# Performance work log

Measured on AMD Instinct MI355X. Metric: run time of the kernel, lower is better.

The kernel has to match this reference:

```python
import jax, jax.numpy as jnp
import numpy as np

S = 14          # grid size
B = 2           # boxes per cell
L_COORD = 5.0
L_NOOBJ = 0.5
N_BATCH = 4096
OBJ_PROB = 0.3  # fraction of cells containing an object


def xywh2xyxy(boxes):
    # boxes [..., 4] with (cx, cy, w, h); cx,cy are in grid units -> divide by S
    x, y, w, h = boxes[..., 0], boxes[..., 1], boxes[..., 2], boxes[..., 3]
    return jnp.stack([x / S - 0.5 * w, y / S - 0.5 * h,
                      x / S + 0.5 * w, y / S + 0.5 * h], axis=-1)


def iou_elementwise(b1, b2):
    # b1, b2: [..., 4] in xyxy format; elementwise IoU (the diagonal of compute_iou)
    lt = jnp.maximum(b1[..., :2], b2[..., :2])
    rb = jnp.minimum(b1[..., 2:], b2[..., 2:])
    wh = jnp.maximum(rb - lt, 0.0)
    inter = wh[..., 0] * wh[..., 1]
    area1 = (b1[..., 2] - b1[..., 0]) * (b1[..., 3] - b1[..., 1])
    area2 = (b2[..., 2] - b2[..., 0]) * (b2[..., 3] - b2[..., 1])
    return inter / (area1 + area2 - inter)


def setup_inputs() -> dict:
    key = jax.random.key(0)
    k1, k2, k3, k4 = jax.random.split(key, 4)
    pred_tensor = jax.random.uniform(k1, (N_BATCH, S, S, 30), dtype=jnp.float32)
    target_boxes = jax.random.uniform(k2, (N_BATCH, S, S, 4), dtype=jnp.float32)
    target_cls = jax.random.uniform(k3, (N_BATCH, S, S, 20), dtype=jnp.float32)
    has_object_map = jax.random.bernoulli(k4, OBJ_PROB, (N_BATCH, S, S))
    return {"pred_tensor": pred_tensor, "target_boxes": target_boxes,
            "target_cls": target_cls, "has_object_map": has_object_map}


def reference(pred_tensor, target_boxes, target_cls, has_object_map):
    N = pred_tensor.shape[0]
    dt = pred_tensor.dtype
    obj = has_object_map.astype(dt)          # (N,S,S)
    noobj = 1.0 - obj
    n_obj = jnp.sum(obj)
    n_noobj = jnp.sum(noobj)

    pred_b1 = pred_tensor[..., 0:5]
    pred_b2 = pred_tensor[..., 5:10]
    pred_cls = pred_tensor[..., 10:30]

    # class prediction loss: sum over object cells / batch size
    cls_loss = jnp.sum(obj[..., None] * (pred_cls - target_cls) ** 2) / N

    # no-object loss: gt confidence (and all 5 entries) assumed 0; per-box sum / num noobj cells
    no_obj_loss = L_NOOBJ * (
        jnp.sum(noobj[..., None] * pred_b1 ** 2) +
        jnp.sum(noobj[..., None] * pred_b2 ** 2)) / n_noobj

    # best-of-B box selection via elementwise IoU against the target box
    tgt_xyxy = xywh2xyxy(target_boxes)
    iou1 = iou_elementwise(xywh2xyxy(pred_b1[..., :4]), tgt_xyxy)
    iou2 = iou_elementwise(xywh2xyxy(pred_b2[..., :4]), tgt_xyxy)
    take1 = iou1 >= iou2
    best_boxes = jnp.where(take1[..., None], pred_b1, pred_b2)  # (N,S,S,5)
    best_iou = jnp.where(take1, iou1, iou2)                      # (N,S,S)

    bx, by, bw, bh = (best_boxes[..., i] for i in range(4))
    tx, ty, tw, th = (target_boxes[..., i] for i in range(4))
    reg = (bx - tx) ** 2 + (by - ty) ** 2 + \
          (jnp.sqrt(bw) - jnp.sqrt(tw)) ** 2 + (jnp.sqrt(bh) - jnp.sqrt(th)) ** 2
    reg_loss = jnp.sum(obj * reg) * L_COORD / n_obj

    # containing-object confidence loss; IoU target is detached
    conf_loss = jnp.sum(
        obj * (best_boxes[..., 4] - jax.lax.stop_gradient(best_iou)) ** 2) / n_obj

    total_loss = reg_loss + conf_loss + no_obj_loss + cls_loss
    return total_loss, reg_loss, conf_loss, no_obj_loss, cls_loss
```

## Files before the change

### kernel.cpp

```cpp
#include <hip/hip_runtime.h>

constexpr int NSLOTS = 64;

__global__ void yl_detect_zero(const unsigned int* __restrict__ hmap,
                               double* __restrict__ acc,
                               int* __restrict__ flag) {
    __shared__ int ok[2];
    const int t = threadIdx.x;
    if (t < 2) ok[t] = 1;
    __syncthreads();
    bool vi = true, vf = true;
    for (int i = t; i < 1024; i += 256) {
        const unsigned int d = hmap[i];
        vi = vi && (d == 0u || d == 1u);
        vf = vf && (d == 0u || d == 0x3f800000u);
    }
    if (!vi) atomicAnd(&ok[0], 0);
    if (!vf) atomicAnd(&ok[1], 0);
    for (int i = t; i < NSLOTS * 5; i += 256) acc[i] = 0.0;
    __syncthreads();
    if (t == 0) *flag = ok[0] ? 1 : (ok[1] ? 2 : 0);
}

__global__ __launch_bounds__(256) void yl_main(
    const float* __restrict__ pred, const float* __restrict__ tb,
    const float* __restrict__ tc, const void* __restrict__ hmap,
    const int* __restrict__ flag_p, double* __restrict__ acc, int cells)
{
    const int cell = blockIdx.x * 256 + threadIdx.x;
    float obj = 0.f, s_cls = 0.f, s_no = 0.f, s_reg = 0.f, s_conf = 0.f;

    if (cell < cells) {
        const int flag = *flag_p;
        if (flag == 1)      obj = (float)((const int*)hmap)[cell];
        else if (flag == 2) obj = ((const float*)hmap)[cell];
        else                obj = (float)((const unsigned char*)hmap)[cell];

        float p[30];
        const float2* p2 = reinterpret_cast<const float2*>(pred + (size_t)cell * 30);
        #pragma unroll
        for (int i = 0; i < 15; ++i) { const float2 v = p2[i]; p[2*i] = v.x; p[2*i+1] = v.y; }

        const float4 tbv = reinterpret_cast<const float4*>(tb)[cell];

        float tcl[20];
        const float4* t4 = reinterpret_cast<const float4*>(tc + (size_t)cell * 20);
        #pragma unroll
        for (int i = 0; i < 5; ++i) {
            const float4 v = t4[i];
            tcl[4*i] = v.x; tcl[4*i+1] = v.y; tcl[4*i+2] = v.z; tcl[4*i+3] = v.w;
        }

        float c = 0.f;
        #pragma unroll
        for (int i = 0; i < 20; ++i) { const float d = p[10 + i] - tcl[i]; c += d * d; }
        s_cls = obj * c;

        float nn = 0.f;
        #pragma unroll
        for (int i = 0; i < 10; ++i) nn += p[i] * p[i];
        s_no = (1.f - obj) * nn;

        const float tx1 = tbv.x / 14.f - 0.5f * tbv.z, ty1 = tbv.y / 14.f - 0.5f * tbv.w;
        const float tx2 = tbv.x / 14.f + 0.5f * tbv.z, ty2 = tbv.y / 14.f + 0.5f * tbv.w;
        const float ta  = (tx2 - tx1) * (ty2 - ty1);

        auto iou_f = [&](float x, float y, float w, float h) -> float {
            const float x1 = x / 14.f - 0.5f * w, y1 = y / 14.f - 0.5f * h;
            const float x2 = x / 14.f + 0.5f * w, y2 = y / 14.f + 0.5f * h;
            const float lw = fmaxf(fminf(x2, tx2) - fmaxf(x1, tx1), 0.f);
            const float lh = fmaxf(fminf(y2, ty2) - fmaxf(y1, ty1), 0.f);
            const float inter = lw * lh;
            const float a = (x2 - x1) * (y2 - y1);
            return inter / (a + ta - inter);
        };
        const float iou1 = iou_f(p[0], p[1], p[2], p[3]);
        const float iou2 = iou_f(p[5], p[6], p[7], p[8]);

        const bool take1 = iou1 >= iou2;
        const float bx = take1 ? p[0] : p[5];
        const float by = take1 ? p[1] : p[6];
        const float bw = take1 ? p[2] : p[7];
        const float bh = take1 ? p[3] : p[8];
        const float bc = take1 ? p[4] : p[9];
        const float biou = take1 ? iou1 : iou2;

        const float dx = bx - tbv.x, dy = by - tbv.y;
        const float dw = sqrtf(bw) - sqrtf(tbv.z);
        const float dh = sqrtf(bh) - sqrtf(tbv.w);
        s_reg = obj * (dx * dx + dy * dy + dw * dw + dh * dh);
        const float dc = bc - biou;
        s_conf = obj * dc * dc;
    }

    float vals[5] = {obj, s_cls, s_no, s_reg, s_conf};
    #pragma unroll
    for (int i = 0; i < 5; ++i) {
        float v = vals[i];
        #pragma unroll
        for (int off = 32; off > 0; off >>= 1) v += __shfl_down(v, off);
        vals[i] = v;
    }
    __shared__ float red[4][5];
    const int lane = threadIdx.x & 63, wid = threadIdx.x >> 6;
    if (lane == 0) {
        #pragma unroll
        for (int i = 0; i < 5; ++i) red[wid][i] = vals[i];
    }
    __syncthreads();
    if (threadIdx.x < 5) {
        const float s = red[0][threadIdx.x] + red[1][threadIdx.x]
                      + red[2][threadIdx.x] + red[3][threadIdx.x];
        atomicAdd(&acc[(blockIdx.x & (NSLOTS - 1)) * 5 + threadIdx.x], (double)s);
    }
}

__global__ void yl_finalize(const double* __restrict__ acc, float* __restrict__ out,
                            int cells, int nbatch) {
    const int t = threadIdx.x;
    double v[5];
    #pragma unroll
    for (int i = 0; i < 5; ++i) v[i] = acc[t * 5 + i];
    #pragma unroll
    for (int i = 0; i < 5; ++i) {
        #pragma unroll
        for (int off = 32; off > 0; off >>= 1) v[i] += __shfl_down(v[i], off);
    }
    if (t == 0) {
        const double n_obj = v[0], n_noobj = (double)cells - v[0];
        const float reg_loss  = (float)(v[3] * 5.0 / n_obj);
        const float conf_loss = (float)(v[4] / n_obj);
        const float no_loss   = (float)(0.5 * v[2] / n_noobj);
        const float cls_loss  = (float)(v[1] / (double)nbatch);
        out[1] = reg_loss;
        out[2] = conf_loss;
        out[3] = no_loss;
        out[4] = cls_loss;
        out[0] = reg_loss + conf_loss + no_loss + cls_loss;
    }
}

extern "C" void kernel_launch(void* const* d_in, const int* in_sizes, int n_in,
                              void* d_out, int out_size, void* d_ws, size_t ws_size,
                              hipStream_t stream) {
    const float* pred = (const float*)d_in[0];
    const float* tb   = (const float*)d_in[1];
    const float* tc   = (const float*)d_in[2];
    const void*  hm   = d_in[3];
    const int cells  = in_sizes[3];
    const int nbatch = cells / 196;
    double* acc = (double*)d_ws;
    int* flag   = (int*)((char*)d_ws + NSLOTS * 5 * sizeof(double));

    yl_detect_zero<<<1, 256, 0, stream>>>((const unsigned int*)hm, acc, flag);
    const int blocks = (cells + 255) / 256;
    yl_main<<<blocks, 256, 0, stream>>>(pred, tb, tc, hm, flag, acc, cells);
    yl_finalize<<<1, 64, 0, stream>>>(acc, (float*)d_out, cells, nbatch);
}
```

Before: 206.8 us.

## Split each cell across five threads for coalesced loads and shared-memory box handoff

Each grid cell is now handled by five cooperating threads, each loading a float2 box slice plus a slice of the class predictions and targets. The box values are staged in shared memory so one thread per cell can do the IoU and regression work. This aims to make the strided per-cell loads better coalesced and raise memory-level parallelism. The cost is 640-thread blocks, an extra barrier, and most threads idling during the IoU phase; the detect kernel's scan bound is also clamped to the input size.

```diff
diff --git a/kernel.cpp b/kernel.cpp
--- a/kernel.cpp
+++ b/kernel.cpp
@@ -4,13 +4,13 @@
 
 __global__ void yl_detect_zero(const unsigned int* __restrict__ hmap,
                                double* __restrict__ acc,
-                               int* __restrict__ flag) {
+                               int* __restrict__ flag, int bound) {
     __shared__ int ok[2];
     const int t = threadIdx.x;
     if (t < 2) ok[t] = 1;
     __syncthreads();
     bool vi = true, vf = true;
-    for (int i = t; i < 1024; i += 256) {
+    for (int i = t; i < bound; i += 256) {
         const unsigned int d = hmap[i];
         vi = vi && (d == 0u || d == 1u);
         vf = vf && (d == 0u || d == 0x3f800000u);
@@ -22,13 +22,21 @@
     if (t == 0) *flag = ok[0] ? 1 : (ok[1] ? 2 : 0);
 }
 
-__global__ __launch_bounds__(256) void yl_main(
+__global__ __launch_bounds__(640) void yl_main(
     const float* __restrict__ pred, const float* __restrict__ tb,
     const float* __restrict__ tc, const void* __restrict__ hmap,
     const int* __restrict__ flag_p, double* __restrict__ acc, int cells)
 {
-    const int cell = blockIdx.x * 256 + threadIdx.x;
+    __shared__ float lp[128 * 10];
+    __shared__ float red[10][5];
+
+    const int tl = threadIdx.x;
+    const int cl = tl / 5;
+    const int q  = tl - 5 * cl;
+    const int cell = blockIdx.x * 128 + cl;
+
     float obj = 0.f, s_cls = 0.f, s_no = 0.f, s_reg = 0.f, s_conf = 0.f;
+    float objsum = 0.f;
 
     if (cell < cells) {
         const int flag = *flag_p;
@@ -36,30 +44,27 @@
         else if (flag == 2) obj = ((const float*)hmap)[cell];
         else                obj = (float)((const unsigned char*)hmap)[cell];
 
-        float p[30];
-        const float2* p2 = reinterpret_cast<const float2*>(pred + (size_t)cell * 30);
+        const float* pc = pred + (size_t)cell * 30;
+        const float2 nb = *reinterpret_cast<const float2*>(pc + 2 * q);
+        const float2 ca = *reinterpret_cast<const float2*>(pc + 10 + 4 * q);
+        const float2 cb = *reinterpret_cast<const float2*>(pc + 12 + 4 * q);
+        const float4 tcv = *reinterpret_cast<const float4*>(tc + (size_t)cell * 20 + 4 * q);
+
+        *reinterpret_cast<float2*>(&lp[cl * 10 + 2 * q]) = nb;
+
+        s_no = (1.f - obj) * (nb.x * nb.x + nb.y * nb.y);
+
+        const float d0 = ca.x - tcv.x, d1 = ca.y - tcv.y;
+        const float d2 = cb.x - tcv.z, d3 = cb.y - tcv.w;
+        s_cls = obj * (d0 * d0 + d1 * d1 + d2 * d2 + d3 * d3);
+    }
+    __syncthreads();
+
+    if (q == 0 && cell < cells) {
+        float p[10];
         #pragma unroll
-        for (int i = 0; i < 15; ++i) { const float2 v = p2[i]; p[2*i] = v.x; p[2*i+1] = v.y; }
-
+        for (int k = 0; k < 10; ++k) p[k] = lp[cl * 10 + k];
         const float4 tbv = reinterpret_cast<const float4*>(tb)[cell];
-
-        float tcl[20];
-        const float4* t4 = reinterpret_cast<const float4*>(tc + (size_t)cell * 20);
-        #pragma unroll
-        for (int i = 0; i < 5; ++i) {
-            const float4 v = t4[i];
-            tcl[4*i] = v.x; tcl[4*i+1] = v.y; tcl[4*i+2] = v.z; tcl[4*i+3] = v.w;
-        }
-
-        float c = 0.f;
-        #pragma unroll
-        for (int i = 0; i < 20; ++i) { const float d = p[10 + i] - tcl[i]; c += d * d; }
-        s_cls = obj * c;
-
-        float nn = 0.f;
-        #pragma unroll
-        for (int i = 0; i < 10; ++i) nn += p[i] * p[i];
-        s_no = (1.f - obj) * nn;
 
         const float tx1 = tbv.x / 14.f - 0.5f * tbv.z, ty1 = tbv.y / 14.f - 0.5f * tbv.w;
         const float tx2 = tbv.x / 14.f + 0.5f * tbv.z, ty2 = tbv.y / 14.f + 0.5f * tbv.w;
@@ -91,9 +96,10 @@
         s_reg = obj * (dx * dx + dy * dy + dw * dw + dh * dh);
         const float dc = bc - biou;
         s_conf = obj * dc * dc;
+        objsum = obj;
     }
 
-    float vals[5] = {obj, s_cls, s_no, s_reg, s_conf};
+    float vals[5] = {objsum, s_cls, s_no, s_reg, s_conf};
     #pragma unroll
     for (int i = 0; i < 5; ++i) {
         float v = vals[i];
@@ -101,17 +107,17 @@
         for (int off = 32; off > 0; off >>= 1) v += __shfl_down(v, off);
         vals[i] = v;
     }
-    __shared__ float red[4][5];
-    const int lane = threadIdx.x & 63, wid = threadIdx.x >> 6;
+    const int lane = tl & 63, wid = tl >> 6;
     if (lane == 0) {
         #pragma unroll
         for (int i = 0; i < 5; ++i) red[wid][i] = vals[i];
     }
     __syncthreads();
-    if (threadIdx.x < 5) {
-        const float s = red[0][threadIdx.x] + red[1][threadIdx.x]
-                      + red[2][threadIdx.x] + red[3][threadIdx.x];
-        atomicAdd(&acc[(blockIdx.x & (NSLOTS - 1)) * 5 + threadIdx.x], (double)s);
+    if (tl < 5) {
+        float s = 0.f;
+        #pragma unroll
+        for (int w = 0; w < 10; ++w) s += red[w][tl];
+        atomicAdd(&acc[(blockIdx.x & (NSLOTS - 1)) * 5 + tl], (double)s);
     }
 }
 
@@ -152,8 +158,9 @@
     double* acc = (double*)d_ws;
     int* flag   = (int*)((char*)d_ws + NSLOTS * 5 * sizeof(double));
 
-    yl_detect_zero<<<1, 256, 0, stream>>>((const unsigned int*)hm, acc, flag);
-    const int blocks = (cells + 255) / 256;
-    yl_main<<<blocks, 256, 0, stream>>>(pred, tb, tc, hm, flag, acc, cells);
+    const int bound = cells / 4 < 1024 ? cells / 4 : 1024;
+    yl_detect_zero<<<1, 256, 0, stream>>>((const unsigned int*)hm, acc, flag, bound);
+    const int blocks = (cells + 127) / 128;
+    yl_main<<<blocks, 640, 0, stream>>>(pred, tb, tc, hm, flag, acc, cells);
     yl_finalize<<<1, 64, 0, stream>>>(acc, (float*)d_out, cells, nbatch);
 }
```

New measurement: 211.1 us. 2.1% more time.

## Process two cells per thread with float4 vector loads and 512-thread blocks

Applied to the files above, without the earlier changes.

Each thread now handles a pair of adjacent cells, so the 30-float prediction rows of both cells form 15 aligned float4 loads and the class targets form 10 float4 loads instead of float2 loads. Blocks grow to 512 threads and the shared reduction covers 8 waves. The aim is wider, more efficient memory transactions on this bandwidth-bound loss. The cost is higher register pressure per thread (100 floats of inputs held live), which may lower occupancy. An odd cell count would drop the last cell.

```diff
diff --git a/kernel.cpp b/kernel.cpp
--- a/kernel.cpp
+++ b/kernel.cpp
@@ -4,13 +4,13 @@
 
 __global__ void yl_detect_zero(const unsigned int* __restrict__ hmap,
                                double* __restrict__ acc,
-                               int* __restrict__ flag) {
+                               int* __restrict__ flag, int bound) {
     __shared__ int ok[2];
     const int t = threadIdx.x;
     if (t < 2) ok[t] = 1;
     __syncthreads();
     bool vi = true, vf = true;
-    for (int i = t; i < 1024; i += 256) {
+    for (int i = t; i < bound; i += 256) {
         const unsigned int d = hmap[i];
         vi = vi && (d == 0u || d == 1u);
         vf = vf && (d == 0u || d == 0x3f800000u);
@@ -22,78 +22,105 @@
     if (t == 0) *flag = ok[0] ? 1 : (ok[1] ? 2 : 0);
 }
 
-__global__ __launch_bounds__(256) void yl_main(
+__device__ __forceinline__ float iou_one(float x, float y, float w, float h,
+                                         float tx1, float ty1, float tx2, float ty2,
+                                         float ta) {
+    const float x1 = x / 14.f - 0.5f * w, y1 = y / 14.f - 0.5f * h;
+    const float x2 = x / 14.f + 0.5f * w, y2 = y / 14.f + 0.5f * h;
+    const float lw = fmaxf(fminf(x2, tx2) - fmaxf(x1, tx1), 0.f);
+    const float lh = fmaxf(fminf(y2, ty2) - fmaxf(y1, ty1), 0.f);
+    const float inter = lw * lh;
+    const float a = (x2 - x1) * (y2 - y1);
+    return inter / (a + ta - inter);
+}
+
+__device__ __forceinline__ void cell_box(
+    float obj, float4 tbv,
+    float p0, float p1, float p2, float p3, float p4,
+    float p5, float p6, float p7, float p8, float p9,
+    float& s_reg, float& s_conf)
+{
+    const float tx1 = tbv.x / 14.f - 0.5f * tbv.z, ty1 = tbv.y / 14.f - 0.5f * tbv.w;
+    const float tx2 = tbv.x / 14.f + 0.5f * tbv.z, ty2 = tbv.y / 14.f + 0.5f * tbv.w;
+    const float ta  = (tx2 - tx1) * (ty2 - ty1);
+    const float iou1 = iou_one(p0, p1, p2, p3, tx1, ty1, tx2, ty2, ta);
+    const float iou2 = iou_one(p5, p6, p7, p8, tx1, ty1, tx2, ty2, ta);
+    const bool take1 = iou1 >= iou2;
+    const float bx = take1 ? p0 : p5;
+    const float by = take1 ? p1 : p6;
+    const float bw = take1 ? p2 : p7;
+    const float bh = take1 ? p3 : p8;
+    const float bc = take1 ? p4 : p9;
+    const float biou = take1 ? iou1 : iou2;
+    const float dx = bx - tbv.x, dy = by - tbv.y;
+    const float dw = sqrtf(bw) - sqrtf(tbv.z);
+    const float dh = sqrtf(bh) - sqrtf(tbv.w);
+    s_reg  += obj * (dx * dx + dy * dy + dw * dw + dh * dh);
+    const float dc = bc - biou;
+    s_conf += obj * dc * dc;
+}
+
+__global__ __launch_bounds__(512) void yl_main(
     const float* __restrict__ pred, const float* __restrict__ tb,
     const float* __restrict__ tc, const void* __restrict__ hmap,
-    const int* __restrict__ flag_p, double* __restrict__ acc, int cells)
+    const int* __restrict__ flag_p, double* __restrict__ acc, int pairs)
 {
-    const int cell = blockIdx.x * 256 + threadIdx.x;
-    float obj = 0.f, s_cls = 0.f, s_no = 0.f, s_reg = 0.f, s_conf = 0.f;
+    const int t = blockIdx.x * 512 + threadIdx.x;
+    float s_obj = 0.f, s_cls = 0.f, s_no = 0.f, s_reg = 0.f, s_conf = 0.f;
 
-    if (cell < cells) {
+    if (t < pairs) {
         const int flag = *flag_p;
-        if (flag == 1)      obj = (float)((const int*)hmap)[cell];
-        else if (flag == 2) obj = ((const float*)hmap)[cell];
-        else                obj = (float)((const unsigned char*)hmap)[cell];
 
-        float p[30];
-        const float2* p2 = reinterpret_cast<const float2*>(pred + (size_t)cell * 30);
+        float4 P[15];
+        const float4* gp = reinterpret_cast<const float4*>(pred) + (size_t)t * 15;
         #pragma unroll
-        for (int i = 0; i < 15; ++i) { const float2 v = p2[i]; p[2*i] = v.x; p[2*i+1] = v.y; }
+        for (int i = 0; i < 15; ++i) P[i] = gp[i];
+        float4 C[10];
+        const float4* gc = reinterpret_cast<const float4*>(tc) + (size_t)t * 10;
+        #pragma unroll
+        for (int i = 0; i < 10; ++i) C[i] = gc[i];
+        const float4* gb = reinterpret_cast<const float4*>(tb) + (size_t)t * 2;
+        const float4 TA = gb[0], TBv = gb[1];
 
-        const float4 tbv = reinterpret_cast<const float4*>(tb)[cell];
+        float objA, objB;
+        if (flag == 1)      { const int2 h = ((const int2*)hmap)[t];   objA = (float)h.x; objB = (float)h.y; }
+        else if (flag == 2) { const float2 h = ((const float2*)hmap)[t]; objA = h.x; objB = h.y; }
+        else                { const uchar2 h = ((const uchar2*)hmap)[t]; objA = (float)h.x; objB = (float)h.y; }
 
-        float tcl[20];
-        const float4* t4 = reinterpret_cast<const float4*>(tc + (size_t)cell * 20);
+        float f[60];
         #pragma unroll
-        for (int i = 0; i < 5; ++i) {
-            const float4 v = t4[i];
-            tcl[4*i] = v.x; tcl[4*i+1] = v.y; tcl[4*i+2] = v.z; tcl[4*i+3] = v.w;
+        for (int i = 0; i < 15; ++i) {
+            f[4*i] = P[i].x; f[4*i+1] = P[i].y; f[4*i+2] = P[i].z; f[4*i+3] = P[i].w;
+        }
+        float g[40];
+        #pragma unroll
+        for (int i = 0; i < 10; ++i) {
+            g[4*i] = C[i].x; g[4*i+1] = C[i].y; g[4*i+2] = C[i].z; g[4*i+3] = C[i].w;
         }
 
-        float c = 0.f;
+        float clsA = 0.f, clsB = 0.f;
         #pragma unroll
-        for (int i = 0; i < 20; ++i) { const float d = p[10 + i] - tcl[i]; c += d * d; }
-        s_cls = obj * c;
+        for (int j = 0; j < 20; ++j) {
+            const float da = f[10 + j] - g[j];      clsA += da * da;
+            const float db = f[40 + j] - g[20 + j]; clsB += db * db;
+        }
+        float noA = 0.f, noB = 0.f;
+        #pragma unroll
+        for (int i = 0; i < 10; ++i) {
+            noA += f[i] * f[i];
+            noB += f[30 + i] * f[30 + i];
+        }
+        s_cls = objA * clsA + objB * clsB;
+        s_no  = (1.f - objA) * noA + (1.f - objB) * noB;
+        s_obj = objA + objB;
 
-        float nn = 0.f;
-        #pragma unroll
-        for (int i = 0; i < 10; ++i) nn += p[i] * p[i];
-        s_no = (1.f - obj) * nn;
-
-        const float tx1 = tbv.x / 14.f - 0.5f * tbv.z, ty1 = tbv.y / 14.f - 0.5f * tbv.w;
-        const float tx2 = tbv.x / 14.f + 0.5f * tbv.z, ty2 = tbv.y / 14.f + 0.5f * tbv.w;
-        const float ta  = (tx2 - tx1) * (ty2 - ty1);
-
-        auto iou_f = [&](float x, float y, float w, float h) -> float {
-            const float x1 = x / 14.f - 0.5f * w, y1 = y / 14.f - 0.5f * h;
-            const float x2 = x / 14.f + 0.5f * w, y2 = y / 14.f + 0.5f * h;
-            const float lw = fmaxf(fminf(x2, tx2) - fmaxf(x1, tx1), 0.f);
-            const float lh = fmaxf(fminf(y2, ty2) - fmaxf(y1, ty1), 0.f);
-            const float inter = lw * lh;
-            const float a = (x2 - x1) * (y2 - y1);
-            return inter / (a + ta - inter);
-        };
-        const float iou1 = iou_f(p[0], p[1], p[2], p[3]);
-        const float iou2 = iou_f(p[5], p[6], p[7], p[8]);
-
-        const bool take1 = iou1 >= iou2;
-        const float bx = take1 ? p[0] : p[5];
-        const float by = take1 ? p[1] : p[6];
-        const float bw = take1 ? p[2] : p[7];
-        const float bh = take1 ? p[3] : p[8];
-        const float bc = take1 ? p[4] : p[9];
-        const float biou = take1 ? iou1 : iou2;
-
-        const float dx = bx - tbv.x, dy = by - tbv.y;
-        const float dw = sqrtf(bw) - sqrtf(tbv.z);
-        const float dh = sqrtf(bh) - sqrtf(tbv.w);
-        s_reg = obj * (dx * dx + dy * dy + dw * dw + dh * dh);
-        const float dc = bc - biou;
-        s_conf = obj * dc * dc;
+        cell_box(objA, TA,  f[0],  f[1],  f[2],  f[3],  f[4],
+                            f[5],  f[6],  f[7],  f[8],  f[9],  s_reg, s_conf);
+        cell_box(objB, TBv, f[30], f[31], f[32], f[33], f[34],
+                            f[35], f[36], f[37], f[38], f[39], s_reg, s_conf);
     }
 
-    float vals[5] = {obj, s_cls, s_no, s_reg, s_conf};
+    float vals[5] = {s_obj, s_cls, s_no, s_reg, s_conf};
     #pragma unroll
     for (int i = 0; i < 5; ++i) {
         float v = vals[i];
@@ -101,7 +128,7 @@
         for (int off = 32; off > 0; off >>= 1) v += __shfl_down(v, off);
         vals[i] = v;
     }
-    __shared__ float red[4][5];
+    __shared__ float red[8][5];
     const int lane = threadIdx.x & 63, wid = threadIdx.x >> 6;
     if (lane == 0) {
         #pragma unroll
@@ -109,8 +136,9 @@
     }
     __syncthreads();
     if (threadIdx.x < 5) {
-        const float s = red[0][threadIdx.x] + red[1][threadIdx.x]
-                      + red[2][threadIdx.x] + red[3][threadIdx.x];
+        float s = 0.f;
+        #pragma unroll
+        for (int w = 0; w < 8; ++w) s += red[w][threadIdx.x];
         atomicAdd(&acc[(blockIdx.x & (NSLOTS - 1)) * 5 + threadIdx.x], (double)s);
     }
 }
@@ -149,11 +177,13 @@
     const void*  hm   = d_in[3];
     const int cells  = in_sizes[3];
     const int nbatch = cells / 196;
+    const int pairs  = cells / 2;
     double* acc = (double*)d_ws;
     int* flag   = (int*)((char*)d_ws + NSLOTS * 5 * sizeof(double));
 
-    yl_detect_zero<<<1, 256, 0, stream>>>((const unsigned int*)hm, acc, flag);
-    const int blocks = (cells + 255) / 256;
-    yl_main<<<blocks, 256, 0, stream>>>(pred, tb, tc, hm, flag, acc, cells);
+    const int bound = cells / 4 < 1024 ? cells / 4 : 1024;
+    yl_detect_zero<<<1, 256, 0, stream>>>((const unsigned int*)hm, acc, flag, bound);
+    const int blocks = (pairs + 511) / 512;
+    yl_main<<<blocks, 512, 0, stream>>>(pred, tb, tc, hm, flag, acc, pairs);
     yl_finalize<<<1, 64, 0, stream>>>(acc, (float*)d_out, cells, nbatch);
 }
```

After: 212.0 us. 2.5% more time.
